# Kernel tuning notes

Measured on AMD Instinct MI355X. Metric: run time of the kernel, lower is better.

Reference implementation:

```python
import jax, jax.numpy as jnp
import numpy as np

INPUT_DIM = 256
HIDDEN_DIM = 128
N = 16384


def setup_inputs() -> dict:
    key = jax.random.key(0)
    k_h, k_wq, k_bq, k_wk, k_bk = jax.random.split(key, 5)
    s = 1.0 / np.sqrt(INPUT_DIM)
    return {
        "H": jax.random.normal(k_h, (N, INPUT_DIM), dtype=jnp.float32),
        "Wq": jax.random.uniform(k_wq, (INPUT_DIM, HIDDEN_DIM), jnp.float32, -s, s),
        "bq": jax.random.uniform(k_bq, (HIDDEN_DIM,), jnp.float32, -s, s),
        "Wk": jax.random.uniform(k_wk, (INPUT_DIM, HIDDEN_DIM), jnp.float32, -s, s),
        "bk": jax.random.uniform(k_bk, (HIDDEN_DIM,), jnp.float32, -s, s),
    }


def reference(H, Wq, bq, Wk, bk):
    n = H.shape[0]
    Q = H @ Wq + bq                      # [N, hidden]
    K = H @ Wk + bk                      # [N, hidden]
    A = Q @ K.T                          # [N, N]
    # zero the diagonal BEFORE scaling/softmax (faithful to torch.where(eye,...))
    A = jnp.where(jnp.eye(n, dtype=bool), jnp.float32(0.0), A)
    A = A / jnp.sqrt(jnp.float32(K.shape[-1]))
    A = jax.nn.softmax(A, axis=-1)
    return A @ H + H                     # [N, T]
```

## Files before the change

### kernel.cpp

```cpp
#include <hip/hip_runtime.h>
#include <hip/hip_bf16.h>

#define NROWS 16384
#define DIN   256
#define DH    128
#define SPLITS 4
#define KVSPL  4096
#define KVBLK  64
#define NIT    (KVSPL / KVBLK)
#define QBLK   256

typedef __attribute__((ext_vector_type(8)))  short  short8;
typedef __attribute__((ext_vector_type(4)))  float  f32x4;
typedef __attribute__((ext_vector_type(16))) float  f32x16;
typedef __attribute__((ext_vector_type(4)))  unsigned short u16x4;
typedef __attribute__((ext_vector_type(4)))  unsigned int   u32x4;

__device__ __forceinline__ unsigned short f2bf(float f) {
  unsigned int u = __float_as_uint(f);
  unsigned int r = (u + 0x7FFFu + ((u >> 16) & 1u)) >> 16;
  return (unsigned short)r;
}
__device__ __forceinline__ float bf2f(unsigned short b) {
  return __uint_as_float(((unsigned int)b) << 16);
}

__device__ __forceinline__ void gload_lds16(const void* g, void* l) {
  __builtin_amdgcn_global_load_lds(
      (const __attribute__((address_space(1))) unsigned int*)g,
      (__attribute__((address_space(3))) unsigned int*)l, 16, 0, 0);
}

__global__ void prep_w(const float* __restrict__ Wq, const float* __restrict__ Wk,
                       unsigned short* __restrict__ WqT, unsigned short* __restrict__ WkT) {
  const float* W = blockIdx.x ? Wk : Wq;
  unsigned short* WT = blockIdx.x ? WkT : WqT;
  int c = threadIdx.x;
  for (int k = 0; k < DIN; ++k)
    WT[c * DIN + k] = f2bf(W[k * DH + c]);
}

__global__ __launch_bounds__(128) void prep_hqk(
    const float* __restrict__ H,
    const unsigned short* __restrict__ WqT, const float* __restrict__ bq,
    const unsigned short* __restrict__ WkT, const float* __restrict__ bk,
    unsigned short* __restrict__ HbT,
    unsigned short* __restrict__ Qb, unsigned short* __restrict__ Kb) {
  __shared__ __align__(16) unsigned short tile[32][264];
  const int tid = threadIdx.x;
  const int qbase = blockIdx.x * 32;

  for (int i = tid; i < 32 * 64; i += 128) {
    int r = i >> 6, c4 = i & 63;
    const f32x4 v = *reinterpret_cast<const f32x4*>(H + (size_t)(qbase + r) * DIN + c4 * 4);
    u16x4 b;
    b[0] = f2bf(v[0]); b[1] = f2bf(v[1]); b[2] = f2bf(v[2]); b[3] = f2bf(v[3]);
    *reinterpret_cast<u16x4*>(&tile[r][c4 * 4]) = b;
  }
  __syncthreads();

  for (int i = tid; i < 256 * 4; i += 128) {
    int c = i >> 2, seg = i & 3;
    short8 t;
#pragma unroll
    for (int j = 0; j < 8; ++j) t[j] = (short)tile[seg * 8 + j][c];
    *reinterpret_cast<short8*>(HbT + (size_t)c * NROWS + qbase + seg * 8) = t;
  }

  const int lane = tid & 63, w = tid >> 6;
  const int col = lane & 15, grp = lane >> 4;

  short8 ah[8];
#pragma unroll
  for (int c = 0; c < 8; ++c)
    ah[c] = *reinterpret_cast<const short8*>(&tile[w * 16 + col][c * 32 + grp * 8]);

  f32x4 accq[8], acck[8];
#pragma unroll
  for (int ct = 0; ct < 8; ++ct) { accq[ct] = f32x4{0,0,0,0}; acck[ct] = f32x4{0,0,0,0}; }

#pragma unroll
  for (int ct = 0; ct < 8; ++ct) {
#pragma unroll
    for (int c = 0; c < 8; ++c) {
      short8 bwq = *reinterpret_cast<const short8*>(WqT + (size_t)(ct * 16 + col) * DIN + c * 32 + grp * 8);
      accq[ct] = __builtin_amdgcn_mfma_f32_16x16x32_bf16(ah[c], bwq, accq[ct], 0, 0, 0);
      short8 bwk = *reinterpret_cast<const short8*>(WkT + (size_t)(ct * 16 + col) * DIN + c * 32 + grp * 8);
      acck[ct] = __builtin_amdgcn_mfma_f32_16x16x32_bf16(ah[c], bwk, acck[ct], 0, 0, 0);
    }
  }

  const float QSCALE = 0.12751742f;
#pragma unroll
  for (int ct = 0; ct < 8; ++ct) {
    float vbq = bq[ct * 16 + col];
    float vbk = bk[ct * 16 + col];
#pragma unroll
    for (int r = 0; r < 4; ++r) {
      int row = qbase + w * 16 + grp * 4 + r;
      Qb[(size_t)row * DH + ct * 16 + col] = f2bf((accq[ct][r] + vbq) * QSCALE);
      Kb[(size_t)row * DH + ct * 16 + col] = f2bf(acck[ct][r] + vbk);
    }
  }
}

__global__ __launch_bounds__(512, 2) void attn_fa(
    const unsigned short* __restrict__ Qb, const unsigned short* __restrict__ Kb,
    const unsigned short* __restrict__ HbT,
    unsigned short* __restrict__ Opart, float* __restrict__ Lp) {
  __shared__ __align__(16) char lds[99328];
  char* KtC = lds;
  char* VtC = lds + 32768;
  float* LsmF = (float*)(lds + 98304);

  const int tid = threadIdx.x;
  const int lane = tid & 63, w = tid >> 6;
  const int l31 = lane & 31, hi = lane >> 5;
  const int swz = (lane & 7) << 4;

  const int sp = blockIdx.x & 3;
  const int qb = blockIdx.x >> 2;
  const int qrow0 = qb * QBLK + w * 32;
  const int kv0 = sp * KVSPL;

  int koff[2];
#pragma unroll
  for (int s = 0; s < 2; ++s) {
    int kvl = (w * 2 + s) * 4 + (lane >> 4);
    int byt = (lane & 15) * 16;
    koff[s] = kvl * DH + ((byt ^ ((kvl & 7) << 4)) >> 1);
  }
  size_t voff[4];
#pragma unroll
  for (int s = 0; s < 4; ++s) {
    int d = (w * 4 + s) * 8 + (lane >> 3);
    int byt = (lane & 7) * 16;
    voff[s] = (size_t)d * NROWS + ((byt ^ ((d & 7) << 4)) >> 1);
  }

  short8 qf[8];
#pragma unroll
  for (int c = 0; c < 8; ++c)
    qf[c] = *reinterpret_cast<const short8*>(Qb + (size_t)(qrow0 + l31) * DH + c * 16 + hi * 8);

  f32x16 acc[8];
#pragma unroll
  for (int dt = 0; dt < 8; ++dt) acc[dt] = {};
  float lsum = 0.f;

  {
    const unsigned short* kbsrc = Kb + (size_t)kv0 * DH;
#pragma unroll
    for (int s = 0; s < 2; ++s)
      gload_lds16(kbsrc + koff[s], KtC + (w * 2 + s) * 1024);
#pragma unroll
    for (int s = 0; s < 4; ++s)
      gload_lds16(HbT + voff[s] + kv0, VtC + (w * 4 + s) * 1024);
  }

  const int dlv = l31 - 4 * hi;

  for (int it = 0; it < NIT; ++it) {
    const int pb = it & 1;
    char* Krd = KtC + pb * 16384;
    char* Vrd = VtC + pb * 32768;
    char* Kwr = KtC + (pb ^ 1) * 16384;
    char* Vwr = VtC + (pb ^ 1) * 32768;
    const int kvbase = kv0 + it * KVBLK;
    const int kvnext = kvbase + KVBLK;

    {
      const unsigned short* kbsrc = Kb + (size_t)kvnext * DH;
#pragma unroll
      for (int s = 0; s < 2; ++s)
        gload_lds16(kbsrc + koff[s], Kwr + (w * 2 + s) * 1024);
#pragma unroll
      for (int s = 0; s < 4; ++s)
        gload_lds16(HbT + voff[s] + kvnext, Vwr + (w * 4 + s) * 1024);
    }

    asm volatile("s_waitcnt vmcnt(6)" ::: "memory");
    __builtin_amdgcn_s_barrier();
    __builtin_amdgcn_sched_barrier(0);

    f32x16 p0 = {}, p1 = {};
#pragma unroll
    for (int c = 0; c < 8; ++c) {
      const int off = (c * 32 + hi * 16) ^ swz;
      short8 ka0 = *reinterpret_cast<const short8*>(Krd + l31 * 256 + off);
      short8 ka1 = *reinterpret_cast<const short8*>(Krd + 8192 + l31 * 256 + off);
      p0 = __builtin_amdgcn_mfma_f32_32x32x16_bf16(ka0, qf[c], p0, 0, 0, 0);
      p1 = __builtin_amdgcn_mfma_f32_32x32x16_bf16(ka1, qf[c], p1, 0, 0, 0);
    }

    const unsigned dq = (unsigned)(qrow0 - kvbase);
    if (dq < 64u) {
      if (dq == 0) {
#pragma unroll
        for (int r = 0; r < 16; ++r)
          if (dlv == ((r & 3) + 8 * (r >> 2))) p0[r] = 0.f;
      } else {
#pragma unroll
        for (int r = 0; r < 16; ++r)
          if (dlv == ((r & 3) + 8 * (r >> 2))) p1[r] = 0.f;
      }
    }

#pragma unroll
    for (int r = 0; r < 16; ++r) { p0[r] = exp2f(p0[r]); lsum += p0[r]; }
#pragma unroll
    for (int r = 0; r < 16; ++r) { p1[r] = exp2f(p1[r]); lsum += p1[r]; }

    unsigned int W[16];
#pragma unroll
    for (int j = 0; j < 8; ++j) {
      asm("v_cvt_pk_bf16_f32 %0, %1, %2" : "=v"(W[j])     : "v"(p0[2*j]), "v"(p0[2*j+1]));
      asm("v_cvt_pk_bf16_f32 %0, %1, %2" : "=v"(W[8 + j]) : "v"(p1[2*j]), "v"(p1[2*j+1]));
    }
#pragma unroll
    for (int b = 0; b < 4; ++b) {
      asm("v_permlane32_swap_b32 %0, %1" : "+v"(W[b*4+0]), "+v"(W[b*4+2]));
      asm("v_permlane32_swap_b32 %0, %1" : "+v"(W[b*4+1]), "+v"(W[b*4+3]));
    }

#pragma unroll
    for (int kc = 0; kc < 4; ++kc) {
      u32x4 paw = { W[kc*4+0], W[kc*4+1], W[kc*4+2], W[kc*4+3] };
      short8 pa = __builtin_bit_cast(short8, paw);
      const int off = (kc * 32 + hi * 16) ^ swz;
#pragma unroll
      for (int dt = 0; dt < 8; ++dt) {
        short8 bv = *reinterpret_cast<const short8*>(Vrd + (dt * 32 + l31) * 128 + off);
        acc[dt] = __builtin_amdgcn_mfma_f32_32x32x16_bf16(pa, bv, acc[dt], 0, 0, 0);
      }
    }

    __builtin_amdgcn_sched_barrier(0);
    __builtin_amdgcn_s_barrier();
  }

  lsum += __shfl_xor(lsum, 32);
  if (lane < 32) LsmF[w * 32 + l31] = lsum;
  asm volatile("s_waitcnt lgkmcnt(0)" ::: "memory");
  __builtin_amdgcn_sched_barrier(0);

  float rl[16];
#pragma unroll
  for (int r = 0; r < 16; ++r)
    rl[r] = 1.0f / LsmF[w * 32 + ((r & 3) + 8 * (r >> 2) + 4 * hi)];

  const size_t obase = (size_t)sp * NROWS * DIN;
#pragma unroll
  for (int dt = 0; dt < 8; ++dt) {
#pragma unroll
    for (int r = 0; r < 16; ++r) {
      int q = qrow0 + (r & 3) + 8 * (r >> 2) + 4 * hi;
      Opart[obase + (size_t)q * DIN + dt * 32 + l31] = f2bf(acc[dt][r] * rl[r]);
    }
  }
  if (lane < 32) Lp[(size_t)sp * NROWS + qrow0 + l31] = lsum;
}

__global__ __launch_bounds__(256) void merge_split(
    const unsigned short* __restrict__ Opart, const float* __restrict__ Lp,
    const float* __restrict__ H, float* __restrict__ out) {
  const int row = blockIdx.x * 16 + (threadIdx.x >> 4);
  const int d0 = (threadIdx.x & 15) * 16;

  float ls[SPLITS], Wt = 0.f;
#pragma unroll
  for (int s = 0; s < SPLITS; ++s) {
    ls[s] = Lp[(size_t)s * NROWS + row];
    Wt += ls[s];
  }
  float invW = 1.0f / Wt;

  float acc[16];
#pragma unroll
  for (int j = 0; j < 16; ++j) acc[j] = 0.f;
#pragma unroll
  for (int s = 0; s < SPLITS; ++s) {
    const unsigned short* p = Opart + ((size_t)s * NROWS + row) * DIN + d0;
#pragma unroll
    for (int h = 0; h < 2; ++h) {
      short8 v = *reinterpret_cast<const short8*>(p + h * 8);
#pragma unroll
      for (int j = 0; j < 8; ++j) acc[h * 8 + j] += ls[s] * bf2f((unsigned short)v[j]);
    }
  }
  const float* hrow = H + (size_t)row * DIN + d0;
  float* orow = out + (size_t)row * DIN + d0;
#pragma unroll
  for (int q = 0; q < 4; ++q) {
    f32x4 hv = *reinterpret_cast<const f32x4*>(hrow + q * 4);
    f32x4 ov;
#pragma unroll
    for (int j = 0; j < 4; ++j) ov[j] = acc[q * 4 + j] * invW + hv[j];
    *reinterpret_cast<f32x4*>(orow + q * 4) = ov;
  }
}

extern "C" void kernel_launch(void* const* d_in, const int* in_sizes, int n_in,
                              void* d_out, int out_size, void* d_ws, size_t ws_size,
                              hipStream_t stream) {
  const float* H  = (const float*)d_in[0];
  const float* Wq = (const float*)d_in[1];
  const float* bq = (const float*)d_in[2];
  const float* Wk = (const float*)d_in[3];
  const float* bk = (const float*)d_in[4];
  float* out = (float*)d_out;

  char* ws = (char*)d_ws;
  unsigned short* HbT   = (unsigned short*)(ws);
  unsigned short* Qb    = (unsigned short*)(ws + 8388608);
  unsigned short* Kb    = (unsigned short*)(ws + 12582912);
  unsigned short* WqT   = (unsigned short*)(ws + 16777216);
  unsigned short* WkT   = (unsigned short*)(ws + 16842752);
  unsigned short* Opart = (unsigned short*)(ws + 20971520);
  float*          Lp    = (float*)(ws + 54525952);

  prep_w<<<2, 128, 0, stream>>>(Wq, Wk, WqT, WkT);
  prep_hqk<<<512, 128, 0, stream>>>(H, WqT, bq, WkT, bk, HbT, Qb, Kb);
  attn_fa<<<256, 512, 0, stream>>>(Qb, Kb, HbT, Opart, Lp);
  merge_split<<<1024, 256, 0, stream>>>(Opart, Lp, H, out);
}
```

Baseline: 318.7 us.

## Restructure attention tiling: 64 query rows per wave, split head dim across blocks

The attention kernel now has each wave own 64 query rows in two 32-row groups that share one K fragment load. The output dimension is split in half across blocks, the KV tile shrinks to 32, and workgroups shrink to 256 threads with a small LDS footprint. Softmax partials are written unnormalized, so the merge sums them directly and the LDS row-sum exchange goes away. MFMA sections are wrapped in setprio, and the prep kernel processes 64 rows per block. Splitting the head dimension recomputes QK^T twice per query tile, and shorter KV blocks add more barriers per unit of work.

```diff
diff --git a/kernel.cpp b/kernel.cpp
--- a/kernel.cpp
+++ b/kernel.cpp
@@ -6,7 +6,7 @@
 #define DH    128
 #define SPLITS 4
 #define KVSPL  4096
-#define KVBLK  64
+#define KVBLK  32
 #define NIT    (KVSPL / KVBLK)
 #define QBLK   256
 
@@ -40,17 +40,17 @@
     WT[c * DIN + k] = f2bf(W[k * DH + c]);
 }
 
-__global__ __launch_bounds__(128) void prep_hqk(
+__global__ __launch_bounds__(256) void prep_hqk(
     const float* __restrict__ H,
     const unsigned short* __restrict__ WqT, const float* __restrict__ bq,
     const unsigned short* __restrict__ WkT, const float* __restrict__ bk,
     unsigned short* __restrict__ HbT,
     unsigned short* __restrict__ Qb, unsigned short* __restrict__ Kb) {
-  __shared__ __align__(16) unsigned short tile[32][264];
+  __shared__ __align__(16) unsigned short tile[64][264];
   const int tid = threadIdx.x;
-  const int qbase = blockIdx.x * 32;
-
-  for (int i = tid; i < 32 * 64; i += 128) {
+  const int qbase = blockIdx.x * 64;
+
+  for (int i = tid; i < 64 * 64; i += 256) {
     int r = i >> 6, c4 = i & 63;
     const f32x4 v = *reinterpret_cast<const f32x4*>(H + (size_t)(qbase + r) * DIN + c4 * 4);
     u16x4 b;
@@ -59,8 +59,8 @@
   }
   __syncthreads();
 
-  for (int i = tid; i < 256 * 4; i += 128) {
-    int c = i >> 2, seg = i & 3;
+  for (int i = tid; i < 256 * 8; i += 256) {
+    int c = i >> 3, seg = i & 7;
     short8 t;
 #pragma unroll
     for (int j = 0; j < 8; ++j) t[j] = (short)tile[seg * 8 + j][c];
@@ -104,161 +104,163 @@
   }
 }
 
-__global__ __launch_bounds__(512, 2) void attn_fa(
+__global__ __launch_bounds__(256, 2) void attn_fa(
     const unsigned short* __restrict__ Qb, const unsigned short* __restrict__ Kb,
     const unsigned short* __restrict__ HbT,
     unsigned short* __restrict__ Opart, float* __restrict__ Lp) {
-  __shared__ __align__(16) char lds[99328];
+  __shared__ __align__(16) char lds[32768];
   char* KtC = lds;
-  char* VtC = lds + 32768;
-  float* LsmF = (float*)(lds + 98304);
+  char* VtC = lds + 16384;
 
   const int tid = threadIdx.x;
   const int lane = tid & 63, w = tid >> 6;
   const int l31 = lane & 31, hi = lane >> 5;
-  const int swz = (lane & 7) << 4;
+  const int kswz = (l31 & 7) << 4;
+  const int vswz = ((l31 >> 1) & 3) << 4;
+  const int dlv = l31 - 4 * hi;
 
   const int sp = blockIdx.x & 3;
-  const int qb = blockIdx.x >> 2;
-  const int qrow0 = qb * QBLK + w * 32;
+  const int dh = (blockIdx.x >> 2) & 1;
+  const int qb = blockIdx.x >> 3;
+  const int qrow0 = qb * QBLK + w * 64;
   const int kv0 = sp * KVSPL;
 
-  int koff[2];
+  int krow[2], kcol[2];
 #pragma unroll
   for (int s = 0; s < 2; ++s) {
-    int kvl = (w * 2 + s) * 4 + (lane >> 4);
-    int byt = (lane & 15) * 16;
-    koff[s] = kvl * DH + ((byt ^ ((kvl & 7) << 4)) >> 1);
-  }
-  size_t voff[4];
-#pragma unroll
-  for (int s = 0; s < 4; ++s) {
-    int d = (w * 4 + s) * 8 + (lane >> 3);
-    int byt = (lane & 7) * 16;
-    voff[s] = (size_t)d * NROWS + ((byt ^ ((d & 7) << 4)) >> 1);
-  }
-
-  short8 qf[8];
-#pragma unroll
-  for (int c = 0; c < 8; ++c)
-    qf[c] = *reinterpret_cast<const short8*>(Qb + (size_t)(qrow0 + l31) * DH + c * 16 + hi * 8);
-
-  f32x16 acc[8];
-#pragma unroll
-  for (int dt = 0; dt < 8; ++dt) acc[dt] = {};
-  float lsum = 0.f;
-
-  {
-    const unsigned short* kbsrc = Kb + (size_t)kv0 * DH;
-#pragma unroll
-    for (int s = 0; s < 2; ++s)
-      gload_lds16(kbsrc + koff[s], KtC + (w * 2 + s) * 1024);
-#pragma unroll
-    for (int s = 0; s < 4; ++s)
-      gload_lds16(HbT + voff[s] + kv0, VtC + (w * 4 + s) * 1024);
-  }
-
-  const int dlv = l31 - 4 * hi;
+    int kv = w * 8 + s * 4 + (lane >> 4);
+    krow[s] = kv;
+    kcol[s] = (((lane & 15) * 16) ^ ((kv & 7) << 4)) >> 1;
+  }
+  int vrow[2], vcol[2];
+#pragma unroll
+  for (int s = 0; s < 2; ++s) {
+    int d = w * 32 + s * 16 + (lane >> 2);
+    vrow[s] = dh * 128 + d;
+    vcol[s] = (((lane & 3) * 16) ^ (((d >> 1) & 3) << 4)) >> 1;
+  }
+
+  short8 qfa[8], qfb[8];
+#pragma unroll
+  for (int c = 0; c < 8; ++c) {
+    qfa[c] = *reinterpret_cast<const short8*>(Qb + (size_t)(qrow0 + l31) * DH + c * 16 + hi * 8);
+    qfb[c] = *reinterpret_cast<const short8*>(Qb + (size_t)(qrow0 + 32 + l31) * DH + c * 16 + hi * 8);
+  }
+
+  f32x16 acc[2][4];
+#pragma unroll
+  for (int g = 0; g < 2; ++g)
+#pragma unroll
+    for (int dt = 0; dt < 4; ++dt) acc[g][dt] = {};
+  float lsa = 0.f, lsb = 0.f;
+
+#pragma unroll
+  for (int s = 0; s < 2; ++s)
+    gload_lds16(Kb + (size_t)(kv0 + krow[s]) * DH + kcol[s], KtC + w * 2048 + s * 1024);
+#pragma unroll
+  for (int s = 0; s < 2; ++s)
+    gload_lds16(HbT + (size_t)vrow[s] * NROWS + kv0 + vcol[s], VtC + w * 2048 + s * 1024);
 
   for (int it = 0; it < NIT; ++it) {
-    const int pb = it & 1;
-    char* Krd = KtC + pb * 16384;
-    char* Vrd = VtC + pb * 32768;
-    char* Kwr = KtC + (pb ^ 1) * 16384;
-    char* Vwr = VtC + (pb ^ 1) * 32768;
+    const int buf = it & 1;
     const int kvbase = kv0 + it * KVBLK;
     const int kvnext = kvbase + KVBLK;
-
-    {
-      const unsigned short* kbsrc = Kb + (size_t)kvnext * DH;
-#pragma unroll
-      for (int s = 0; s < 2; ++s)
-        gload_lds16(kbsrc + koff[s], Kwr + (w * 2 + s) * 1024);
-#pragma unroll
-      for (int s = 0; s < 4; ++s)
-        gload_lds16(HbT + voff[s] + kvnext, Vwr + (w * 4 + s) * 1024);
-    }
-
-    asm volatile("s_waitcnt vmcnt(6)" ::: "memory");
+    char* Kwr = KtC + (buf ^ 1) * 8192;
+    char* Vwr = VtC + (buf ^ 1) * 8192;
+
+#pragma unroll
+    for (int s = 0; s < 2; ++s)
+      gload_lds16(Kb + (size_t)(kvnext + krow[s]) * DH + kcol[s], Kwr + w * 2048 + s * 1024);
+#pragma unroll
+    for (int s = 0; s < 2; ++s)
+      gload_lds16(HbT + (size_t)vrow[s] * NROWS + kvnext + vcol[s], Vwr + w * 2048 + s * 1024);
+
+    asm volatile("s_waitcnt vmcnt(4)" ::: "memory");
     __builtin_amdgcn_s_barrier();
     __builtin_amdgcn_sched_barrier(0);
 
-    f32x16 p0 = {}, p1 = {};
+    const char* Krd = KtC + buf * 8192;
+    f32x16 pa = {}, pb = {};
+    __builtin_amdgcn_s_setprio(1);
 #pragma unroll
     for (int c = 0; c < 8; ++c) {
-      const int off = (c * 32 + hi * 16) ^ swz;
-      short8 ka0 = *reinterpret_cast<const short8*>(Krd + l31 * 256 + off);
-      short8 ka1 = *reinterpret_cast<const short8*>(Krd + 8192 + l31 * 256 + off);
-      p0 = __builtin_amdgcn_mfma_f32_32x32x16_bf16(ka0, qf[c], p0, 0, 0, 0);
-      p1 = __builtin_amdgcn_mfma_f32_32x32x16_bf16(ka1, qf[c], p1, 0, 0, 0);
-    }
-
-    const unsigned dq = (unsigned)(qrow0 - kvbase);
-    if (dq < 64u) {
-      if (dq == 0) {
-#pragma unroll
-        for (int r = 0; r < 16; ++r)
-          if (dlv == ((r & 3) + 8 * (r >> 2))) p0[r] = 0.f;
-      } else {
-#pragma unroll
-        for (int r = 0; r < 16; ++r)
-          if (dlv == ((r & 3) + 8 * (r >> 2))) p1[r] = 0.f;
+      short8 ka = *reinterpret_cast<const short8*>(Krd + l31 * 256 + ((c * 32 + hi * 16) ^ kswz));
+      pa = __builtin_amdgcn_mfma_f32_32x32x16_bf16(ka, qfa[c], pa, 0, 0, 0);
+      pb = __builtin_amdgcn_mfma_f32_32x32x16_bf16(ka, qfb[c], pb, 0, 0, 0);
+    }
+    __builtin_amdgcn_s_setprio(0);
+
+    if (qrow0 == kvbase) {
+#pragma unroll
+      for (int r = 0; r < 16; ++r)
+        if (dlv == ((r & 3) + 8 * (r >> 2))) pa[r] = 0.f;
+    }
+    if (qrow0 + 32 == kvbase) {
+#pragma unroll
+      for (int r = 0; r < 16; ++r)
+        if (dlv == ((r & 3) + 8 * (r >> 2))) pb[r] = 0.f;
+    }
+
+#pragma unroll
+    for (int r = 0; r < 16; ++r) { pa[r] = exp2f(pa[r]); lsa += pa[r]; }
+#pragma unroll
+    for (int r = 0; r < 16; ++r) { pb[r] = exp2f(pb[r]); lsb += pb[r]; }
+
+    unsigned int Wa[8], Wb[8];
+#pragma unroll
+    for (int j = 0; j < 8; ++j) {
+      asm("v_cvt_pk_bf16_f32 %0, %1, %2" : "=v"(Wa[j]) : "v"(pa[2*j]), "v"(pa[2*j+1]));
+      asm("v_cvt_pk_bf16_f32 %0, %1, %2" : "=v"(Wb[j]) : "v"(pb[2*j]), "v"(pb[2*j+1]));
+    }
+#pragma unroll
+    for (int b = 0; b < 2; ++b) {
+      asm("v_permlane32_swap_b32 %0, %1" : "+v"(Wa[b*4+0]), "+v"(Wa[b*4+2]));
+      asm("v_permlane32_swap_b32 %0, %1" : "+v"(Wa[b*4+1]), "+v"(Wa[b*4+3]));
+      asm("v_permlane32_swap_b32 %0, %1" : "+v"(Wb[b*4+0]), "+v"(Wb[b*4+2]));
+      asm("v_permlane32_swap_b32 %0, %1" : "+v"(Wb[b*4+1]), "+v"(Wb[b*4+3]));
+    }
+
+    const char* Vrd = VtC + buf * 8192;
+    __builtin_amdgcn_s_setprio(1);
+#pragma unroll
+    for (int kc = 0; kc < 2; ++kc) {
+      u32x4 wa = { Wa[kc*4+0], Wa[kc*4+1], Wa[kc*4+2], Wa[kc*4+3] };
+      u32x4 wb = { Wb[kc*4+0], Wb[kc*4+1], Wb[kc*4+2], Wb[kc*4+3] };
+      short8 paf = __builtin_bit_cast(short8, wa);
+      short8 pbf = __builtin_bit_cast(short8, wb);
+      const int off = (kc * 32 + hi * 16) ^ vswz;
+#pragma unroll
+      for (int dt = 0; dt < 4; ++dt) {
+        short8 bv = *reinterpret_cast<const short8*>(Vrd + (dt * 32 + l31) * 64 + off);
+        acc[0][dt] = __builtin_amdgcn_mfma_f32_32x32x16_bf16(paf, bv, acc[0][dt], 0, 0, 0);
+        acc[1][dt] = __builtin_amdgcn_mfma_f32_32x32x16_bf16(pbf, bv, acc[1][dt], 0, 0, 0);
       }
     }
-
-#pragma unroll
-    for (int r = 0; r < 16; ++r) { p0[r] = exp2f(p0[r]); lsum += p0[r]; }
-#pragma unroll
-    for (int r = 0; r < 16; ++r) { p1[r] = exp2f(p1[r]); lsum += p1[r]; }
-
-    unsigned int W[16];
-#pragma unroll
-    for (int j = 0; j < 8; ++j) {
-      asm("v_cvt_pk_bf16_f32 %0, %1, %2" : "=v"(W[j])     : "v"(p0[2*j]), "v"(p0[2*j+1]));
-      asm("v_cvt_pk_bf16_f32 %0, %1, %2" : "=v"(W[8 + j]) : "v"(p1[2*j]), "v"(p1[2*j+1]));
-    }
-#pragma unroll
-    for (int b = 0; b < 4; ++b) {
-      asm("v_permlane32_swap_b32 %0, %1" : "+v"(W[b*4+0]), "+v"(W[b*4+2]));
-      asm("v_permlane32_swap_b32 %0, %1" : "+v"(W[b*4+1]), "+v"(W[b*4+3]));
-    }
-
-#pragma unroll
-    for (int kc = 0; kc < 4; ++kc) {
-      u32x4 paw = { W[kc*4+0], W[kc*4+1], W[kc*4+2], W[kc*4+3] };
-      short8 pa = __builtin_bit_cast(short8, paw);
-      const int off = (kc * 32 + hi * 16) ^ swz;
-#pragma unroll
-      for (int dt = 0; dt < 8; ++dt) {
-        short8 bv = *reinterpret_cast<const short8*>(Vrd + (dt * 32 + l31) * 128 + off);
-        acc[dt] = __builtin_amdgcn_mfma_f32_32x32x16_bf16(pa, bv, acc[dt], 0, 0, 0);
-      }
-    }
+    __builtin_amdgcn_s_setprio(0);
 
     __builtin_amdgcn_sched_barrier(0);
     __builtin_amdgcn_s_barrier();
   }
 
-  lsum += __shfl_xor(lsum, 32);
-  if (lane < 32) LsmF[w * 32 + l31] = lsum;
-  asm volatile("s_waitcnt lgkmcnt(0)" ::: "memory");
-  __builtin_amdgcn_sched_barrier(0);
-
-  float rl[16];
-#pragma unroll
-  for (int r = 0; r < 16; ++r)
-    rl[r] = 1.0f / LsmF[w * 32 + ((r & 3) + 8 * (r >> 2) + 4 * hi)];
+  lsa += __shfl_xor(lsa, 32);
+  lsb += __shfl_xor(lsb, 32);
 
   const size_t obase = (size_t)sp * NROWS * DIN;
-#pragma unroll
-  for (int dt = 0; dt < 8; ++dt) {
+  const int colb = dh * 128;
+#pragma unroll
+  for (int dt = 0; dt < 4; ++dt) {
 #pragma unroll
     for (int r = 0; r < 16; ++r) {
       int q = qrow0 + (r & 3) + 8 * (r >> 2) + 4 * hi;
-      Opart[obase + (size_t)q * DIN + dt * 32 + l31] = f2bf(acc[dt][r] * rl[r]);
-    }
-  }
-  if (lane < 32) Lp[(size_t)sp * NROWS + qrow0 + l31] = lsum;
+      int cc = colb + dt * 32 + l31;
+      Opart[obase + (size_t)q * DIN + cc] = f2bf(acc[0][dt][r]);
+      Opart[obase + (size_t)(q + 32) * DIN + cc] = f2bf(acc[1][dt][r]);
+    }
+  }
+  if (dh == 0 && lane < 32) {
+    Lp[(size_t)sp * NROWS + qrow0 + l31] = lsa;
+    Lp[(size_t)sp * NROWS + qrow0 + 32 + l31] = lsb;
+  }
 }
 
 __global__ __launch_bounds__(256) void merge_split(
@@ -267,12 +269,9 @@
   const int row = blockIdx.x * 16 + (threadIdx.x >> 4);
   const int d0 = (threadIdx.x & 15) * 16;
 
-  float ls[SPLITS], Wt = 0.f;
-#pragma unroll
-  for (int s = 0; s < SPLITS; ++s) {
-    ls[s] = Lp[(size_t)s * NROWS + row];
-    Wt += ls[s];
-  }
+  float Wt = 0.f;
+#pragma unroll
+  for (int s = 0; s < SPLITS; ++s) Wt += Lp[(size_t)s * NROWS + row];
   float invW = 1.0f / Wt;
 
   float acc[16];
@@ -285,7 +284,7 @@
     for (int h = 0; h < 2; ++h) {
       short8 v = *reinterpret_cast<const short8*>(p + h * 8);
 #pragma unroll
-      for (int j = 0; j < 8; ++j) acc[h * 8 + j] += ls[s] * bf2f((unsigned short)v[j]);
+      for (int j = 0; j < 8; ++j) acc[h * 8 + j] += bf2f((unsigned short)v[j]);
     }
   }
   const float* hrow = H + (size_t)row * DIN + d0;
@@ -320,7 +319,7 @@
   float*          Lp    = (float*)(ws + 54525952);
 
   prep_w<<<2, 128, 0, stream>>>(Wq, Wk, WqT, WkT);
-  prep_hqk<<<512, 128, 0, stream>>>(H, WqT, bq, WkT, bk, HbT, Qb, Kb);
-  attn_fa<<<256, 512, 0, stream>>>(Qb, Kb, HbT, Opart, Lp);
+  prep_hqk<<<256, 256, 0, stream>>>(H, WqT, bq, WkT, bk, HbT, Qb, Kb);
+  attn_fa<<<512, 256, 0, stream>>>(Qb, Kb, HbT, Opart, Lp);
   merge_split<<<1024, 256, 0, stream>>>(Opart, Lp, H, out);
 }
```

Result: slower. 424.3 us (+33.1%).
